# Optimization experiments

Hardware: AMD Instinct MI355X
Metric: run time of the kernel (lower is better)

The kernel has to match this reference:

```python
import jax, jax.numpy as jnp
import numpy as np

WINDOW_SIZE = 11
SIGMA = 1.5


def _gaussian_window(window_size, sigma, channel, dtype):
    xs = np.arange(window_size, dtype=np.float64)
    g = np.exp(-((xs - window_size // 2) ** 2) / (2.0 * sigma ** 2))
    g = (g / g.sum()).astype(np.float32)
    w2d = np.outer(g, g)  # [K, K]
    # depthwise kernel: [channel, 1, K, K] (OIHW with feature_group_count=channel)
    w = np.broadcast_to(w2d[None, None], (channel, 1, window_size, window_size))
    return jnp.asarray(np.ascontiguousarray(w), dtype=dtype)


def _depthwise_conv(img, window, channel):
    pad = WINDOW_SIZE // 2
    return jax.lax.conv_general_dilated(
        img, window,
        window_strides=(1, 1),
        padding=((pad, pad), (pad, pad)),
        dimension_numbers=("NCHW", "OIHW", "NCHW"),
        feature_group_count=channel,
    )


def setup_inputs() -> dict:
    key = jax.random.key(0)
    k1, k2 = jax.random.split(key)
    x = jax.random.uniform(k1, (16, 3, 512, 512), dtype=jnp.float32)
    y = jax.random.uniform(k2, (16, 3, 512, 512), dtype=jnp.float32)
    return {"x": x, "y": y}


def reference(x, y):
    channel = x.shape[1]
    window = _gaussian_window(WINDOW_SIZE, SIGMA, channel, x.dtype)

    mu_x = _depthwise_conv(x, window, channel)
    mu_y = _depthwise_conv(y, window, channel)
    mu_x_sq = mu_x * mu_x
    mu_y_sq = mu_y * mu_y
    mu_xy = mu_x * mu_y

    sigma_x = _depthwise_conv(x * x, window, channel) - mu_x_sq
    sigma_y = _depthwise_conv(y * y, window, channel) - mu_y_sq
    sigma_xy = _depthwise_conv(x * y, window, channel) - mu_xy

    C1 = 0.01 ** 2
    C2 = 0.03 ** 2
    ssim_n = (2.0 * mu_xy + C1) * (2.0 * sigma_xy + C2)
    ssim_d = (mu_x_sq + mu_y_sq + C1) * (sigma_x + sigma_y + C2)
    ssim_map = ssim_n / (ssim_d + 1e-08)
    # size_average=True
    return jnp.mean(ssim_map)
```

## Files before the change

kernel.cpp:

```cpp
#include <hip/hip_runtime.h>
#include <cmath>

constexpr int IMG_H = 512;
constexpr int IMG_W = 512;
constexpr int PLANES = 48;
constexpr int R_OUT = 8;
constexpr int BANDS = IMG_H / R_OUT;
constexpr int PSTR = 512;
constexpr int NSLOT = 64;
constexpr int NBLK = PLANES * BANDS;
constexpr long long TOTAL_PIX = (long long)PLANES * IMG_H * IMG_W;

struct GWin { float g[11]; };

__device__ __forceinline__ int swzd(int d) { return d ^ (((d >> 5) & 7) << 2); }
__device__ __forceinline__ int swzd4(int b) { return b ^ ((b >> 3) & 7); }

template<bool CHK>
__device__ __forceinline__ float2 ld2(const float* __restrict__ base, int gr, int c0) {
    if (CHK && (unsigned)gr >= (unsigned)IMG_H) return make_float2(0.f, 0.f);
    return *(const float2*)(base + (size_t)gr * IMG_W + c0);
}

__device__ __forceinline__ float hpass8(const float* __restrict__ fr0,
                                        int l, const int (&pb)[6],
                                        const GWin& win) {
    float m[4][8];
#pragma unroll
    for (int f = 0; f < 4; ++f) {
        const float* fr = fr0 + f * PSTR;
        float w24[24];
#pragma unroll
        for (int B = 0; B < 6; ++B) {
            const float4 v = *(const float4*)&fr[pb[B]];
            w24[4 * B + 0] = v.x;  w24[4 * B + 1] = v.y;
            w24[4 * B + 2] = v.z;  w24[4 * B + 3] = v.w;
        }
        if (l == 0)  { w24[3] = w24[4] = w24[5] = w24[6] = w24[7] = 0.f; }
        if (l == 63) { w24[16] = w24[17] = w24[18] = w24[19] = w24[20] = 0.f; }
#pragma unroll
        for (int j = 0; j < 8; ++j) {
            float s = 0.f;
#pragma unroll
            for (int k = 0; k < 11; ++k) s += win.g[k] * w24[j + 3 + k];
            m[f][j] = s;
        }
    }
    float ls = 0.f;
#pragma unroll
    for (int u = 0; u < 8; ++u) {
        const float sb  = m[0][u];
        const float db  = m[1][u];
        const float css = m[2][u];
        const float cdd = m[3][u];
        const float A = sb * sb;
        const float B = db * db;
        const float C1 = 0.01f * 0.01f;
        const float C2 = 0.03f * 0.03f;
        const float n1 = 0.5f * (A - B) + C1;
        const float n2 = 0.5f * ((css - cdd) - (A - B)) + C2;
        const float d1 = 0.5f * (A + B) + C1;
        const float d2 = 0.5f * ((css + cdd) - (A + B)) + C2;
        ls += (n1 * n2) * __builtin_amdgcn_rcpf(d1 * d2 + 1e-8f);
    }
    return ls;
}

template<int I0>
__device__ __forceinline__ void vconv4(const float2 (&xr)[18], const float2 (&yr)[18],
                                       float* __restrict__ hb, int pws,
                                       const GWin& win) {
    float2 acc[4][4];
#pragma unroll
    for (int j = 0; j < 4; ++j)
#pragma unroll
        for (int f = 0; f < 4; ++f) acc[j][f] = make_float2(0.f, 0.f);
#pragma unroll
    for (int k = 0; k < 14; ++k) {
        const float2 xv = xr[I0 + k], yv = yr[I0 + k];
        const float2 sv = make_float2(xv.x + yv.x, xv.y + yv.y);
        const float2 dv = make_float2(xv.x - yv.x, xv.y - yv.y);
        const float2 ssv = make_float2(sv.x * sv.x, sv.y * sv.y);
        const float2 ddv = make_float2(dv.x * dv.x, dv.y * dv.y);
#pragma unroll
        for (int j = 0; j < 4; ++j) {
            const int t = k - j;
            if (t >= 0 && t <= 10) {
                const float g = win.g[t];
                acc[j][0].x += g * sv.x;   acc[j][0].y += g * sv.y;
                acc[j][1].x += g * dv.x;   acc[j][1].y += g * dv.y;
                acc[j][2].x += g * ssv.x;  acc[j][2].y += g * ssv.y;
                acc[j][3].x += g * ddv.x;  acc[j][3].y += g * ddv.y;
            }
        }
    }
#pragma unroll
    for (int j = 0; j < 4; ++j)
#pragma unroll
        for (int f = 0; f < 4; ++f)
            *(float2*)&hb[(j * 4 + f) * PSTR + pws] = acc[j][f];
}

template<bool CHK>
__device__ __forceinline__ float band_body(const float* __restrict__ xp,
                                           const float* __restrict__ yp,
                                           int r0, int c0, int tid,
                                           float* __restrict__ hb,
                                           const GWin& win)
{
    const int pws = swzd(2 * tid);
    const int row = tid >> 6, l = tid & 63;
    int pb[6];
#pragma unroll
    for (int B = 0; B < 6; ++B) {
        int blk = 2 * l - 2 + B;
        blk = blk < 0 ? 0 : (blk > 127 ? 127 : blk);
        pb[B] = 4 * swzd4(blk);
    }

    float2 xr[18], yr[18];
#pragma unroll
    for (int i = 0; i < 14; ++i) {
        xr[i] = ld2<CHK>(xp, r0 - 5 + i, c0);
        yr[i] = ld2<CHK>(yp, r0 - 5 + i, c0);
    }

    vconv4<0>(xr, yr, hb, pws, win);
    __syncthreads();

#pragma unroll
    for (int i = 14; i < 18; ++i) {
        xr[i] = ld2<CHK>(xp, r0 - 5 + i, c0);
        yr[i] = ld2<CHK>(yp, r0 - 5 + i, c0);
    }

    float lsum = hpass8(hb + row * 4 * PSTR, l, pb, win);
    __syncthreads();

    vconv4<4>(xr, yr, hb, pws, win);
    __syncthreads();

    lsum += hpass8(hb + row * 4 * PSTR, l, pb, win);
    return lsum;
}

__global__ __launch_bounds__(256)
void ssim_sd_kernel(const float* __restrict__ x,
                    const float* __restrict__ y,
                    double* __restrict__ accum,
                    GWin win)
{
    __shared__ __align__(16) float hbuf[4 * 4 * PSTR];

    const int tid = threadIdx.x;
    const int bid = blockIdx.x;
    const int L   = (bid & 7) * (NBLK / 8) + (bid >> 3);
    const int band  = L & (BANDS - 1);
    const int plane = L >> 6;
    const int r0    = band * R_OUT;
    const int c0    = tid * 2;

    const float* __restrict__ xp = x + (size_t)plane * (IMG_H * IMG_W);
    const float* __restrict__ yp = y + (size_t)plane * (IMG_H * IMG_W);

    float lsum;
    if (band >= 1 && band <= BANDS - 2)
        lsum = band_body<false>(xp, yp, r0, c0, tid, hbuf, win);
    else
        lsum = band_body<true>(xp, yp, r0, c0, tid, hbuf, win);

#pragma unroll
    for (int off = 32; off; off >>= 1) lsum += __shfl_down(lsum, off);
    if ((tid & 63) == 0) {
        const int wid = L * 4 + (tid >> 6);
        atomicAdd(&accum[(wid & (NSLOT - 1)) * 8], (double)lsum);
    }
}

__global__ __launch_bounds__(64)
void ssim_finalize_kernel(const double* __restrict__ accum,
                          float* __restrict__ out)
{
    const int l = threadIdx.x;
    double s = accum[l * 8];
#pragma unroll
    for (int off = 32; off; off >>= 1) s += __shfl_down(s, off);
    if (l == 0) out[0] = (float)(s / (double)TOTAL_PIX);
}

extern "C" void kernel_launch(void* const* d_in, const int* in_sizes, int n_in,
                              void* d_out, int out_size, void* d_ws, size_t ws_size,
                              hipStream_t stream) {
    const float* x = (const float*)d_in[0];
    const float* y = (const float*)d_in[1];
    float* out = (float*)d_out;
    double* accum = (double*)d_ws;

    GWin win;
    {
        double g[11], s = 0.0;
        for (int i = 0; i < 11; ++i) {
            double d = (double)i - 5.0;
            g[i] = std::exp(-(d * d) / (2.0 * 1.5 * 1.5));
            s += g[i];
        }
        for (int i = 0; i < 11; ++i) win.g[i] = (float)(g[i] / s);
    }

    (void)hipMemsetAsync(d_ws, 0, NSLOT * 8 * sizeof(double), stream);

    ssim_sd_kernel<<<NBLK, 256, 0, stream>>>(x, y, accum, win);
    ssim_finalize_kernel<<<1, 64, 0, stream>>>(accum, out);
}
```

Baseline: 60.11 us.

## Process 16 output rows per block with a ring-buffered register row window

Each block now covers 16 output rows instead of 8. Input rows are kept in an 18-entry register ring buffer so four vertical-pass chunks can reuse rows as new ones are loaded. This cuts the 10-row halo reload overhead per band roughly in half and halves the block count. In exchange there are more sync stages per block, more register pressure, and fewer blocks (1536) to fill the GPU.

```diff
diff --git a/kernel.cpp b/kernel.cpp
--- a/kernel.cpp
+++ b/kernel.cpp
@@ -4,7 +4,7 @@
 constexpr int IMG_H = 512;
 constexpr int IMG_W = 512;
 constexpr int PLANES = 48;
-constexpr int R_OUT = 8;
+constexpr int R_OUT = 16;
 constexpr int BANDS = IMG_H / R_OUT;
 constexpr int PSTR = 512;
 constexpr int NSLOT = 64;
@@ -67,9 +67,9 @@
 }
 
 template<int I0>
-__device__ __forceinline__ void vconv4(const float2 (&xr)[18], const float2 (&yr)[18],
-                                       float* __restrict__ hb, int pws,
-                                       const GWin& win) {
+__device__ __forceinline__ void vconv4m(const float2 (&xr)[18], const float2 (&yr)[18],
+                                        float* __restrict__ hb, int pws,
+                                        const GWin& win) {
     float2 acc[4][4];
 #pragma unroll
     for (int j = 0; j < 4; ++j)
@@ -77,7 +77,8 @@
         for (int f = 0; f < 4; ++f) acc[j][f] = make_float2(0.f, 0.f);
 #pragma unroll
     for (int k = 0; k < 14; ++k) {
-        const float2 xv = xr[I0 + k], yv = yr[I0 + k];
+        const int s = (I0 + k) % 18;
+        const float2 xv = xr[s], yv = yr[s];
         const float2 sv = make_float2(xv.x + yv.x, xv.y + yv.y);
         const float2 dv = make_float2(xv.x - yv.x, xv.y - yv.y);
         const float2 ssv = make_float2(sv.x * sv.x, sv.y * sv.y);
@@ -125,7 +126,7 @@
         yr[i] = ld2<CHK>(yp, r0 - 5 + i, c0);
     }
 
-    vconv4<0>(xr, yr, hb, pws, win);
+    vconv4m<0>(xr, yr, hb, pws, win);
     __syncthreads();
 
 #pragma unroll
@@ -133,11 +134,32 @@
         xr[i] = ld2<CHK>(xp, r0 - 5 + i, c0);
         yr[i] = ld2<CHK>(yp, r0 - 5 + i, c0);
     }
-
     float lsum = hpass8(hb + row * 4 * PSTR, l, pb, win);
     __syncthreads();
 
-    vconv4<4>(xr, yr, hb, pws, win);
+    vconv4m<4>(xr, yr, hb, pws, win);
+    __syncthreads();
+
+#pragma unroll
+    for (int i = 0; i < 4; ++i) {
+        xr[i] = ld2<CHK>(xp, r0 + 13 + i, c0);
+        yr[i] = ld2<CHK>(yp, r0 + 13 + i, c0);
+    }
+    lsum += hpass8(hb + row * 4 * PSTR, l, pb, win);
+    __syncthreads();
+
+    vconv4m<8>(xr, yr, hb, pws, win);
+    __syncthreads();
+
+#pragma unroll
+    for (int i = 4; i < 8; ++i) {
+        xr[i] = ld2<CHK>(xp, r0 + 13 + i, c0);
+        yr[i] = ld2<CHK>(yp, r0 + 13 + i, c0);
+    }
+    lsum += hpass8(hb + row * 4 * PSTR, l, pb, win);
+    __syncthreads();
+
+    vconv4m<12>(xr, yr, hb, pws, win);
     __syncthreads();
 
     lsum += hpass8(hb + row * 4 * PSTR, l, pb, win);
@@ -145,10 +167,10 @@
 }
 
 __global__ __launch_bounds__(256)
-void ssim_sd_kernel(const float* __restrict__ x,
-                    const float* __restrict__ y,
-                    double* __restrict__ accum,
-                    GWin win)
+void ssim_q16_kernel(const float* __restrict__ x,
+                     const float* __restrict__ y,
+                     double* __restrict__ accum,
+                     GWin win)
 {
     __shared__ __align__(16) float hbuf[4 * 4 * PSTR];
 
@@ -156,7 +178,7 @@
     const int bid = blockIdx.x;
     const int L   = (bid & 7) * (NBLK / 8) + (bid >> 3);
     const int band  = L & (BANDS - 1);
-    const int plane = L >> 6;
+    const int plane = L >> 5;
     const int r0    = band * R_OUT;
     const int c0    = tid * 2;
 
@@ -209,6 +231,6 @@
 
     (void)hipMemsetAsync(d_ws, 0, NSLOT * 8 * sizeof(double), stream);
 
-    ssim_sd_kernel<<<NBLK, 256, 0, stream>>>(x, y, accum, win);
+    ssim_q16_kernel<<<NBLK, 256, 0, stream>>>(x, y, accum, win);
     ssim_finalize_kernel<<<1, 64, 0, stream>>>(accum, out);
 }
```

New measurement: 75.70 us. 1.26x slower.
